# Optimization experiments

Hardware: AMD Instinct MI355X
Metric: run time of the kernel (lower is better)

The kernel has to match this reference:

```python
import jax, jax.numpy as jnp
import numpy as np
from jax import lax

DN = ('NCHW', 'OIHW', 'NCHW')


def _conv(x, w, b=None, pad='SAME'):
    y = lax.conv_general_dilated(x, w, (1, 1), pad, dimension_numbers=DN)
    return y if b is None else y + b[None, :, None, None]


def setup_inputs() -> dict:
    key = jax.random.key(0)
    ks = jax.random.split(key, 16)
    N, I, H, W = 8, 128, 40, 40
    C, Hc, A, P, O = 256, 256, 256, 256, 256  # in/hidden/attention/projection/out channels
    s = 0.05
    f32 = jnp.float32
    return {
        'x': jax.random.normal(ks[0], (N, I, H, W), f32),
        'h0': jax.random.normal(ks[1], (1, Hc, 1, 1), f32),
        'w_px': jax.random.normal(ks[2], (C, I, 1, 1), f32) * s,
        'b_px': jnp.zeros((C,), f32),
        'w_qx': jax.random.normal(ks[3], (A, C, 3, 3), f32) * s,
        'w_qh': jax.random.normal(ks[4], (A, Hc, 3, 3), f32) * s,
        'w_kx': jax.random.normal(ks[5], (A, C, 3, 3), f32) * (s * A ** -0.5),
        'w_kh': jax.random.normal(ks[6], (A, Hc, 3, 3), f32) * (s * A ** -0.5),
        'w_vx': jax.random.normal(ks[7], (P, C, 3, 3), f32) * s,
        'w_vh': jax.random.normal(ks[8], (P, Hc, 3, 3), f32) * s,
        'w_z': jax.random.normal(ks[9], (Hc, 2 * P, 1, 1), f32) * s,
        'b_z': jnp.ones((Hc,), f32),  # init_gate = 1
        'w_h': jax.random.normal(ks[10], (Hc, 2 * P, 1, 1), f32) * s,
        'b_h': jnp.zeros((Hc,), f32),
        'w_out': jax.random.normal(ks[11], (O, C + 2 * P, 1, 1), f32) * s,
        'b_out': jnp.zeros((O,), f32),
    }


def reference(x, h0, w_px, b_px, w_qx, w_qh, w_kx, w_kh, w_vx, w_vh,
              w_z, b_z, w_h, b_h, w_out, b_out):
    # proj_x: 1x1 conv fusing inputs (single input, groups=1)
    xp = _conv(x, w_px, b_px)
    N, _, H, W = xp.shape
    Q = H * W
    # x-side tokens are step-invariant: compute once
    q_x = _conv(xp, w_qx, pad='SAME').reshape(N, -1, Q)          # [N, A, Q]
    k_x4 = _conv(xp, w_kx, pad='VALID')                           # [N, A, H-2, W-2]
    D = k_x4.shape[2] * k_x4.shape[3]
    k_x = k_x4.reshape(N, -1, D)                                  # [N, A, D]
    v_x = _conv(xp, w_vx, pad='VALID').reshape(N, -1, D)          # [N, P, D]

    def step(h):
        q_h = _conv(h, w_qh, pad='SAME').reshape(N, -1, Q)
        k_h = _conv(h, w_kh, pad='VALID').reshape(N, -1, D)
        v_h = _conv(h, w_vh, pad='VALID').reshape(N, -1, D)
        q = jnp.stack([q_x, q_h], 0)   # [A=2(query src), N, C, Q]
        k = jnp.stack([k_x, k_h], 0)   # [B=2(key src),   N, C, D]
        v = jnp.stack([v_x, v_h], 0)   # [B=2,            N, P, D]
        logits = jnp.einsum('ancq,bncd->anbqd', q, k)   # [2, N, 2, Q, D]
        wt = jax.nn.softmax(logits, axis=-1)
        a = jnp.einsum('bncd,anbqd->anbcq', v, wt)       # [2, N, 2, P, Q]
        a = a.reshape(2, N, -1, H, W)                    # channel layout: (B, P)
        a_x, a_h = a[0], a[1]
        z = jax.nn.sigmoid(_conv(a_h, w_z, b_z))
        h_cand = jnp.tanh(_conv(a_h, w_h, b_h))
        h_new = z * h + (1.0 - z) * h_cand               # dropout p=0 -> identity
        out = _conv(jnp.concatenate([xp, a_x], axis=1), w_out, b_out)
        return out, h_new

    h = jnp.broadcast_to(h0, (N, h0.shape[1], H, W))
    _, h = step(h)          # step 1: builds hidden state
    out, _ = step(h)        # step 2: output depends on recurrent gate
    return out
```

## Files before the change

### kernel.cpp

```cpp
#include <hip/hip_runtime.h>
#include <math.h>


typedef _Float16 f16;
typedef _Float16 h8 __attribute__((ext_vector_type(8)));
typedef __attribute__((ext_vector_type(4))) float f4;

__device__ __forceinline__ ushort f2h(float f) {
  union { f16 h; ushort u; } cv; cv.h = (f16)f; return cv.u;
}
__device__ __forceinline__ float h2f(ushort u) {
  union { ushort u; f16 h; } cv; cv.u = u; return (float)cv.h;
}

struct MgArgs {
  const ushort* A; long sAb;
  const ushort* B; long sBb;
  int M, Nn, K, Krow, mode, gRow0, swap, aConv, bConv;
  const ushort* zp;
  float* Y; long sYb, sYm; int nPer; long sYb2;
  const float* bias; int biasN;
  ushort* Yh; long sYpb, sYpm, pOff;
  ushort* Y2h;
};

__device__ __forceinline__ void mg_body(const MgArgs& g, ushort* lbase)
{
  const int bz = blockIdx.z;
  const ushort* __restrict__ A = g.A + (long)bz * g.sAb;
  const ushort* __restrict__ B = g.B + (long)bz * g.sBb;
  const int mb = g.swap ? blockIdx.y : blockIdx.x;
  const int nb = g.swap ? blockIdx.x : blockIdx.y;
  const int m0 = mb * 64, n0 = nb * 64;
  const int t = threadIdx.x;
  const int lane = t & 63, wv = t >> 6;
  const int r = lane & 15, qd = lane >> 4;
  const int wn = wv * 16;
  const int lrow = lane >> 3, lch = lane & 7;
  f4 acc[4];
  #pragma unroll
  for (int i = 0; i < 4; ++i) acc[i] = (f4){0.f, 0.f, 0.f, 0.f};

  const int cg8 = (lch ^ lrow) * 8;
  int aB[2], aY[2], aX[2]; long aO[2];
  int bB[2], bY[2], bX[2]; long bO[2];
  #pragma unroll
  for (int i = 0; i < 2; ++i) {
    int gr = m0 + wv * 16 + i * 8 + lrow;
    if (g.aConv) {
      int n8 = gr / 1600, pos = gr - n8 * 1600;
      int py = pos / 40, px = pos - py * 40;
      aB[i] = n8 * 1600; aY[i] = py; aX[i] = px;
    } else { if (gr > g.M - 1) gr = g.M - 1; aO[i] = (long)gr * g.Krow; }
  }
  #pragma unroll
  for (int i = 0; i < 2; ++i) {
    int gr = n0 + wv * 16 + i * 8 + lrow;
    if (g.bConv) {
      int n8 = gr / 1600, pos = gr - n8 * 1600;
      int py = pos / 40, px = pos - py * 40;
      bB[i] = n8 * 1600; bY[i] = py; bX[i] = px;
    } else { if (gr > g.Nn - 1) gr = g.Nn - 1; bO[i] = (long)gr * g.Krow; }
  }

  auto stage = [&](int ch, int lb) {
    int cb = ch / 9, tap = ch - cb * 9;
    int tdy = tap / 3 - 1, tdx = tap - (tap / 3) * 3 - 1;
    int kin = cb << 6;
    int kc2 = ch << 6;
    #pragma unroll
    for (int i = 0; i < 2; ++i) {
      const ushort* p; size_t go;
      if (g.aConv) {
        int yy = aY[i] + tdy, xx = aX[i] + tdx;
        bool v = ((unsigned)yy < 40u) && ((unsigned)xx < 40u);
        if (v) { go = (size_t)(aB[i] + yy * 40 + xx) * 768 + kin + cg8; p = A; }
        else   { go = 0; p = g.zp; }
      } else { go = (size_t)(aO[i] + kc2 + cg8); p = A; }
      __builtin_amdgcn_global_load_lds(p + go, lbase + lb + wv * 1024 + i * 512, 16, 0, 0);
    }
    #pragma unroll
    for (int i = 0; i < 2; ++i) {
      const ushort* p; size_t go;
      if (g.bConv) {
        int yy = bY[i] + tdy, xx = bX[i] + tdx;
        bool v = ((unsigned)yy < 40u) && ((unsigned)xx < 40u);
        if (v) { go = (size_t)(bB[i] + yy * 40 + xx) * 768 + kin + cg8; p = B; }
        else   { go = 0; p = g.zp; }
      } else { go = (size_t)(bO[i] + kc2 + cg8); p = B; }
      __builtin_amdgcn_global_load_lds(p + go, lbase + lb + 4096 + wv * 1024 + i * 512, 16, 0, 0);
    }
  };

  auto compute = [&](int lb) {
    #pragma unroll
    for (int kk = 0; kk < 2; ++kk) {
      int off = (((kk << 2) + qd) ^ (r & 7)) << 3;
      h8 af[4], bf;
      #pragma unroll
      for (int mt = 0; mt < 4; ++mt)
        af[mt] = *(const h8*)&lbase[lb + (mt * 16 + r) * 64 + off];
      bf = *(const h8*)&lbase[lb + 4096 + (wn + r) * 64 + off];
      #pragma unroll
      for (int mt = 0; mt < 4; ++mt)
        acc[mt] = __builtin_amdgcn_mfma_f32_16x16x32_f16(af[mt], bf, acc[mt], 0, 0, 0);
    }
  };

  const int nch = g.K >> 6;
  stage(0, 0);
  int ch = 0;
  while (ch + 2 <= nch) {
    stage(ch + 1, 8192);
    asm volatile("s_waitcnt vmcnt(4)" ::: "memory");
    __builtin_amdgcn_s_barrier();
    __builtin_amdgcn_sched_barrier(0);
    compute(0);
    __builtin_amdgcn_s_barrier();
    __builtin_amdgcn_sched_barrier(0);
    if (ch + 2 < nch) {
      stage(ch + 2, 0);
      asm volatile("s_waitcnt vmcnt(4)" ::: "memory");
    } else {
      asm volatile("s_waitcnt vmcnt(0)" ::: "memory");
    }
    __builtin_amdgcn_s_barrier();
    __builtin_amdgcn_sched_barrier(0);
    compute(8192);
    __builtin_amdgcn_s_barrier();
    __builtin_amdgcn_sched_barrier(0);
    ch += 2;
  }
  if (ch < nch) {
    asm volatile("s_waitcnt vmcnt(0)" ::: "memory");
    __builtin_amdgcn_s_barrier();
    __builtin_amdgcn_sched_barrier(0);
    compute(0);
  }

  #pragma unroll
  for (int mt = 0; mt < 4; ++mt) {
    int nn = n0 + wn + r;
    if (nn >= g.Nn) continue;
    #pragma unroll
    for (int e = 0; e < 4; ++e) {
      int mm = m0 + mt * 16 + qd * 4 + e;
      if (mm >= g.M) continue;
      float v = acc[mt][e];
      if (g.mode == 0) {
        if (g.bias) v += g.bias[mm];
        int b2 = nn / g.nPer, nq = nn - b2 * g.nPer;
        g.Y[(size_t)bz * g.sYb + (size_t)b2 * g.sYb2 + (size_t)mm * g.sYm + nq] = v;
      } else if (g.mode == 1) {
        if (g.bias) v += g.bias[g.biasN ? nn : mm];
        g.Yh[(size_t)bz * g.sYpb + (size_t)mm * g.sYpm + nn + g.pOff] = f2h(v);
      } else if (g.mode == 2) {
        int gm = g.gRow0 + mm;
        int n8 = gm / 1600, q = gm - n8 * 1600;
        ushort h = f2h(v);
        if (nn < 256) {
          g.Yh[(size_t)n8 * 409600 + (size_t)q * 256 + nn] = h;
        } else {
          int qy = q / 40, qx = q - qy * 40;
          if (qy >= 1 && qy <= 38 && qx >= 1 && qx <= 38)
            g.Y2h[(size_t)n8 * 369664 + (size_t)((qy - 1) * 38 + qx - 1) * 256 + (nn - 256)] = h;
        }
      } else {
        int gn = g.gRow0 + nn;
        int n8 = gn / 1600, q = gn - n8 * 1600;
        int qy = q / 40, qx = q - qy * 40;
        if (qy >= 1 && qy <= 38 && qx >= 1 && qx <= 38)
          g.Yh[(size_t)n8 * 376832 + (size_t)mm * 1472 + (qy - 1) * 38 + qx - 1] = f2h(v);
      }
    }
  }
}

#define MG_KERN(name) \
__global__ __launch_bounds__(256) void name(MgArgs g) { \
  __shared__ ushort S[16384]; mg_body(g, S); }
MG_KERN(mg_xp)
MG_KERN(mg_v)
MG_KERN(mg_cls)
MG_KERN(mg_lg)
MG_KERN(mg_pv)
MG_KERN(mg_out)
#undef MG_KERN

__global__ __launch_bounds__(256) void mgemm_w(
    const ushort* __restrict__ A, long sAb,
    const ushort* __restrict__ B, long sBb,
    int M, int Nn, int K, int Krow, int mode, int gRow0, int swap,
    int aConv, int bConv,
    const ushort* __restrict__ zp,
    float* __restrict__ Y, long sYb, long sYm, int nPer, long sYb2,
    const float* __restrict__ bias, int biasN,
    ushort* __restrict__ Yh, long sYpb, long sYpm, long pOff,
    ushort* __restrict__ Y2h)
{
  __shared__ ushort S[12288];
  const int bz = blockIdx.z;
  A += (long)bz * sAb;
  B += (long)bz * sBb;
  const int mb = swap ? blockIdx.y : blockIdx.x;
  const int nb = swap ? blockIdx.x : blockIdx.y;
  const int m0 = mb * 64, n0 = nb * 128;
  const int t = threadIdx.x;
  const int lane = t & 63, wv = t >> 6;
  const int r = lane & 15, qd = lane >> 4;
  const int wn = wv * 32;
  const int lrow = lane >> 3, lch = lane & 7;
  f4 acc[4][2];
  #pragma unroll
  for (int i = 0; i < 4; ++i)
    #pragma unroll
    for (int j = 0; j < 2; ++j) acc[i][j] = (f4){0.f, 0.f, 0.f, 0.f};

  const int cg8 = (lch ^ lrow) * 8;
  int aB[2], aY[2], aX[2]; long aO[2];
  int bB[4], bY[4], bX[4]; long bO[4];
  #pragma unroll
  for (int i = 0; i < 2; ++i) {
    int gr = m0 + wv * 16 + i * 8 + lrow;
    if (aConv) {
      int n8 = gr / 1600, pos = gr - n8 * 1600;
      int py = pos / 40, px = pos - py * 40;
      aB[i] = n8 * 1600; aY[i] = py; aX[i] = px;
    } else { if (gr > M - 1) gr = M - 1; aO[i] = (long)gr * Krow; }
  }
  #pragma unroll
  for (int i = 0; i < 4; ++i) {
    int gr = n0 + wv * 32 + i * 8 + lrow;
    if (bConv) {
      int n8 = gr / 1600, pos = gr - n8 * 1600;
      int py = pos / 40, px = pos - py * 40;
      bB[i] = n8 * 1600; bY[i] = py; bX[i] = px;
    } else { if (gr > Nn - 1) gr = Nn - 1; bO[i] = (long)gr * Krow; }
  }

  ushort* lbase = S;
  for (int kc = 0; kc < K; kc += 64) {
    __syncthreads();
    int ch = kc >> 6;
    int cb = ch / 9, tap = ch - cb * 9;
    int tdy = tap / 3 - 1, tdx = tap - (tap / 3) * 3 - 1;
    int kin = cb << 6;
    #pragma unroll
    for (int i = 0; i < 2; ++i) {
      const ushort* p; size_t go;
      if (aConv) {
        int yy = aY[i] + tdy, xx = aX[i] + tdx;
        bool v = ((unsigned)yy < 40u) && ((unsigned)xx < 40u);
        if (v) { go = (size_t)(aB[i] + yy * 40 + xx) * 768 + kin + cg8; p = A; }
        else   { go = 0; p = zp; }
      } else { go = (size_t)(aO[i] + kc + cg8); p = A; }
      __builtin_amdgcn_global_load_lds(p + go, lbase + wv * 1024 + i * 512, 16, 0, 0);
    }
    #pragma unroll
    for (int i = 0; i < 4; ++i) {
      const ushort* p; size_t go;
      if (bConv) {
        int yy = bY[i] + tdy, xx = bX[i] + tdx;
        bool v = ((unsigned)yy < 40u) && ((unsigned)xx < 40u);
        if (v) { go = (size_t)(bB[i] + yy * 40 + xx) * 768 + kin + cg8; p = B; }
        else   { go = 0; p = zp; }
      } else { go = (size_t)(bO[i] + kc + cg8); p = B; }
      __builtin_amdgcn_global_load_lds(p + go, lbase + 4096 + wv * 2048 + i * 512, 16, 0, 0);
    }
    __syncthreads();
    #pragma unroll
    for (int kk = 0; kk < 2; ++kk) {
      int off = (((kk << 2) + qd) ^ (r & 7)) << 3;
      h8 af[4], bf[2];
      #pragma unroll
      for (int mt = 0; mt < 4; ++mt)
        af[mt] = *(const h8*)&lbase[(mt * 16 + r) * 64 + off];
      #pragma unroll
      for (int nt = 0; nt < 2; ++nt)
        bf[nt] = *(const h8*)&lbase[4096 + (wn + nt * 16 + r) * 64 + off];
      #pragma unroll
      for (int mt = 0; mt < 4; ++mt)
        #pragma unroll
        for (int nt = 0; nt < 2; ++nt)
          acc[mt][nt] = __builtin_amdgcn_mfma_f32_16x16x32_f16(af[mt], bf[nt], acc[mt][nt], 0, 0, 0);
    }
  }
  #pragma unroll
  for (int mt = 0; mt < 4; ++mt)
    #pragma unroll
    for (int nt = 0; nt < 2; ++nt) {
      int nn = n0 + wn + nt * 16 + r;
      if (nn >= Nn) continue;
      #pragma unroll
      for (int e = 0; e < 4; ++e) {
        int mm = m0 + mt * 16 + qd * 4 + e;
        if (mm >= M) continue;
        float v = acc[mt][nt][e];
        if (mode == 0) {
          if (bias) v += bias[mm];
          int b2 = nn / nPer, nq = nn - b2 * nPer;
          Y[(size_t)bz * sYb + (size_t)b2 * sYb2 + (size_t)mm * sYm + nq] = v;
        } else if (mode == 1) {
          if (bias) v += bias[biasN ? nn : mm];
          Yh[(size_t)bz * sYpb + (size_t)mm * sYpm + nn + pOff] = f2h(v);
        } else if (mode == 2) {
          int gm = gRow0 + mm;
          int n8 = gm / 1600, q = gm - n8 * 1600;
          ushort h = f2h(v);
          if (nn < 256) {
            Yh[(size_t)n8 * 409600 + (size_t)q * 256 + nn] = h;
          } else {
            int qy = q / 40, qx = q - qy * 40;
            if (qy >= 1 && qy <= 38 && qx >= 1 && qx <= 38)
              Y2h[(size_t)n8 * 369664 + (size_t)((qy - 1) * 38 + qx - 1) * 256 + (nn - 256)] = h;
          }
        } else {
          int gn = gRow0 + nn;
          int n8 = gn / 1600, q = gn - n8 * 1600;
          int qy = q / 40, qx = q - qy * 40;
          if (qy >= 1 && qy <= 38 && qx >= 1 && qx <= 38)
            Yh[(size_t)n8 * 376832 + (size_t)mm * 1472 + (qy - 1) * 38 + qx - 1] = f2h(v);
        }
      }
    }
}

__global__ __launch_bounds__(256) void prep_all(
    const float* __restrict__ x,
    const float* __restrict__ w_qx, const float* __restrict__ w_kx,
    const float* __restrict__ w_vx,
    const float* __restrict__ w_px, const float* __restrict__ w_out,
    const float* __restrict__ w_kh, const float* __restrict__ w_vh,
    const float* __restrict__ w_z, const float* __restrict__ w_h,
    ushort* __restrict__ xT, ushort* __restrict__ Wqk, ushort* __restrict__ Wv,
    ushort* __restrict__ wpx, ushort* __restrict__ wout,
    ushort* __restrict__ Wkv, ushort* __restrict__ Wzh,
    ushort* __restrict__ zp, ushort* __restrict__ vxp)
{
  long gi = (long)blockIdx.x * 256 + threadIdx.x;
  if (gi < 64) zp[gi] = 0;
  long i = gi;
  if (i < 1638400) {
    int i1 = (int)(i & 127); long r = i >> 7;
    int q = (int)(r % 1600); int n8 = (int)(r / 1600);
    xT[i] = f2h(x[(long)n8 * 204800 + (long)i1 * 1600 + q]);
    return;
  }
  i -= 1638400;
  if (i < 1769472) {
    int o = (int)(i / 2304), k = (int)(i - (long)o * 2304);
    int cb = k / 576, rem = k - cb * 576;
    int tap = rem >> 6, ci = rem & 63;
    int si = (cb * 64 + ci) * 9 + tap;
    float f; ushort* d; int oo;
    if (o < 256)      { f = w_qx[o * 2304 + si];         d = Wqk; oo = o; }
    else if (o < 512) { f = w_kx[(o - 256) * 2304 + si]; d = Wqk; oo = o; }
    else              { f = w_vx[(o - 512) * 2304 + si]; d = Wv;  oo = o - 512; }
    d[oo * 2304 + k] = f2h(f);
    return;
  }
  i -= 1769472;
  if (i < 32768)  { wpx[i]  = f2h(w_px[i]);  return; }
  i -= 32768;
  if (i < 196608) { wout[i] = f2h(w_out[i]); return; }
  i -= 196608;
  if (i < 1179648) { Wkv[i] = f2h(i < 589824 ? w_kh[i] : w_vh[i - 589824]); return; }
  i -= 1179648;
  if (i < 262144)  { Wzh[i] = f2h(i < 131072 ? w_z[i] : w_h[i - 131072]); return; }
  i -= 262144;
  if (i < 57344) {
    int j = (int)(i % 28); int rr = (int)(i / 28);
    int c = rr % 256, n = rr / 256;
    vxp[(size_t)n * 376832 + (size_t)c * 1472 + 1444 + j] = 0;
  }
}

__global__ __launch_bounds__(64) void uniform_kv_kern(
    const float* __restrict__ h0, const float* __restrict__ w_qh,
    const float* __restrict__ w_kh, const float* __restrict__ w_vh,
    float* __restrict__ qh1, float* __restrict__ kh1, float* __restrict__ vh1)
{
  int a = blockIdx.x, j = blockIdx.y, t = threadIdx.x;
  const float* wsel = (j < 9) ? w_qh : (j == 9) ? w_kh : w_vh;
  bool dyok0 = true, dyok2 = true, dxok0 = true, dxok2 = true;
  if (j < 9) {
    int uy = j / 3, ux = j - uy * 3;
    dyok0 = (uy != 0); dyok2 = (uy != 2);
    dxok0 = (ux != 0); dxok2 = (ux != 2);
  }
  float acc = 0.f;
  for (int c = t; c < 256; c += 64) {
    const float* wp = wsel + a * 2304 + c * 9;
    float s = 0.f;
    #pragma unroll
    for (int dy = 0; dy < 3; ++dy) {
      if ((dy == 0 && !dyok0) || (dy == 2 && !dyok2)) continue;
      #pragma unroll
      for (int dx = 0; dx < 3; ++dx) {
        if ((dx == 0 && !dxok0) || (dx == 2 && !dxok2)) continue;
        s += wp[dy * 3 + dx];
      }
    }
    acc += s * h0[c];
  }
  #pragma unroll
  for (int o = 32; o; o >>= 1) acc += __shfl_down(acc, o);
  if (t == 0) {
    if (j < 9) qh1[j * 256 + a] = acc;
    else if (j == 9) kh1[a] = acc;
    else vh1[a] = acc;
  }
}

__global__ __launch_bounds__(256) void l0_logits(
    const float* __restrict__ qh1, const ushort* __restrict__ kxT,
    float* __restrict__ L0)
{
  __shared__ float qs[2304];
  int db = blockIdx.x, n = blockIdx.y;
  for (int i = threadIdx.x; i < 2304; i += 256) qs[i] = qh1[i];
  __syncthreads();
  int d = db * 256 + threadIdx.x;
  bool act = d < 1444;
  const ushort* vp = kxT + (size_t)n * 369664 + (act ? (size_t)d * 256 : 0);
  float acc[9] = {0.f,0.f,0.f,0.f,0.f,0.f,0.f,0.f,0.f};
  for (int c8 = 0; c8 < 256; c8 += 8) {
    h8 v = *(const h8*)(const void*)(vp + c8);
    #pragma unroll
    for (int j = 0; j < 8; ++j) {
      float f = (float)v[j];
      #pragma unroll
      for (int u = 0; u < 9; ++u) acc[u] += qs[u * 256 + c8 + j] * f;
    }
  }
  if (act)
    for (int u = 0; u < 9; ++u) L0[n * 12996 + u * 1444 + d] = acc[u];
}

__global__ __launch_bounds__(256) void softmax_rows(float* __restrict__ p, int L)
{
  float* rp = p + (long)blockIdx.x * L;
  int t = threadIdx.x;
  __shared__ float redm[4], reds[4];
  float mx = -3.4e38f;
  for (int i = t; i < L; i += 256) mx = fmaxf(mx, rp[i]);
  #pragma unroll
  for (int o = 32; o; o >>= 1) mx = fmaxf(mx, __shfl_down(mx, o));
  if ((t & 63) == 0) redm[t >> 6] = mx;
  __syncthreads();
  mx = fmaxf(fmaxf(redm[0], redm[1]), fmaxf(redm[2], redm[3]));
  float s = 0.f;
  for (int i = t; i < L; i += 256) { float v = expf(rp[i] - mx); rp[i] = v; s += v; }
  #pragma unroll
  for (int o = 32; o; o >>= 1) s += __shfl_down(s, o);
  if ((t & 63) == 0) reds[t >> 6] = s;
  __syncthreads();
  float inv = 1.f / (reds[0] + reds[1] + reds[2] + reds[3]);
  for (int i = t; i < L; i += 256) rp[i] *= inv;
}

__global__ __launch_bounds__(256) void a10_pv(
    const float* __restrict__ L0, const ushort* __restrict__ vxp,
    float* __restrict__ a10)
{
  int u = blockIdx.x, n = blockIdx.y;
  __shared__ float wts[1472];
  const float* wrow = L0 + n * 12996 + u * 1444;
  for (int i = threadIdx.x; i < 1472; i += 256) wts[i] = (i < 1444) ? wrow[i] : 0.f;
  __syncthreads();
  int p = threadIdx.x;
  const ushort* vp = vxp + (size_t)n * 376832 + (size_t)p * 1472;
  float acc = 0.f;
  for (int d8 = 0; d8 < 1472; d8 += 8) {
    h8 v = *(const h8*)(const void*)(vp + d8);
    #pragma unroll
    for (int j = 0; j < 8; ++j) acc += wts[d8 + j] * (float)v[j];
  }
  a10[n * 2304 + u * 256 + p] = acc;
}

__global__ __launch_bounds__(256) void build_AV(
    const float* __restrict__ a10, const float* __restrict__ vh1,
    ushort* __restrict__ AV)
{
  int i = blockIdx.x * 256 + threadIdx.x;
  if (i >= 72 * 512) return;
  int row = i >> 9, j = i & 511;
  int n = row / 9, u = row - n * 9;
  float f = (j < 256) ? a10[n * 2304 + u * 256 + j] : vh1[j - 256];
  AV[i] = f2h(f);
}

__global__ __launch_bounds__(256) void gate_ew2(
    const float* __restrict__ pre72p, const float* __restrict__ b_z,
    const float* __restrict__ b_h, const float* __restrict__ h0,
    float* __restrict__ h1)
{
  int i = blockIdx.x * 256 + threadIdx.x;
  if (i >= 72 * 256) return;
  int row = i >> 8, c = i & 255;
  float zs = 0.f, hs = 0.f;
  #pragma unroll
  for (int s = 0; s < 4; ++s) {
    zs += pre72p[s * 36864 + row * 512 + c];
    hs += pre72p[s * 36864 + row * 512 + 256 + c];
  }
  float z = 1.f / (1.f + expf(-(zs + b_z[c])));
  float hv = tanhf(hs + b_h[c]);
  int n = row / 9, u = row - n * 9;
  h1[n * 2304 + c * 9 + u] = z * h0[c] + (1.f - z) * hv;
}

__global__ __launch_bounds__(256) void build_GA(
    const float* __restrict__ h1, ushort* __restrict__ GA)
{
  int i = blockIdx.x * 256 + threadIdx.x;
  if (i >= 72 * 2304) return;
  int row = i / 2304, k = i - row * 2304;
  int c = k / 9, tap = k - c * 9;
  int u = row % 9;
  int ty = u / 3, tx = u - ty * 3;
  int dy = tap / 3, dx = tap - dy * 3;
  int uy = (ty == 0) ? (dy == 0 ? 0 : 1) : (ty == 2) ? (dy == 2 ? 2 : 1) : 1;
  int ux = (tx == 0) ? (dx == 0 ? 0 : 1) : (tx == 2) ? (dx == 2 ? 2 : 1) : 1;
  GA[i] = f2h(h1[(row / 9) * 2304 + c * 9 + uy * 3 + ux]);
}

__global__ __launch_bounds__(256) void softmax_h16(
    const ushort* __restrict__ p, ushort* __restrict__ wt)
{
  long row = blockIdx.x;
  const ushort* rp = p + row * 1472;
  ushort* op = wt + row * 1472;
  int t = threadIdx.x;
  __shared__ float buf[1444];
  __shared__ float redm[4], reds[4];
  float mx = -3.4e38f;
  for (int i = t; i < 1444; i += 256) { float v = h2f(rp[i]); buf[i] = v; mx = fmaxf(mx, v); }
  #pragma unroll
  for (int o = 32; o; o >>= 1) mx = fmaxf(mx, __shfl_down(mx, o));
  if ((t & 63) == 0) redm[t >> 6] = mx;
  __syncthreads();
  mx = fmaxf(fmaxf(redm[0], redm[1]), fmaxf(redm[2], redm[3]));
  float s = 0.f;
  for (int i = t; i < 1444; i += 256) { float v = expf(buf[i] - mx); buf[i] = v; s += v; }
  #pragma unroll
  for (int o = 32; o; o >>= 1) s += __shfl_down(s, o);
  if ((t & 63) == 0) reds[t >> 6] = s;
  __syncthreads();
  float inv = 1.f / (reds[0] + reds[1] + reds[2] + reds[3]);
  for (int i = t; i < 1472; i += 256)
    op[i] = f2h((i < 1444) ? buf[i] * inv : 0.f);
}

__global__ __launch_bounds__(256) void attn_b1(
    const ushort* __restrict__ qT, const float* __restrict__ khvcp,
    ushort* __restrict__ xaT)
{
  __shared__ float ks[2304];
  __shared__ float vs[2304];
  __shared__ float es[256][10];
  int n = blockIdx.y;
  int q0 = blockIdx.x * 256;
  for (int i = threadIdx.x; i < 2304; i += 256) {
    int tt = i >> 8, c = i & 255;
    size_t base = (size_t)(n * 9 + tt) * 512;
    float sk = 0.f, sv = 0.f;
    #pragma unroll
    for (int s = 0; s < 6; ++s) {
      sk += khvcp[s * 36864 + base + c];
      sv += khvcp[s * 36864 + base + 256 + c];
    }
    ks[i] = sk; vs[i] = sv;
  }
  __syncthreads();
  int q = q0 + threadIdx.x;
  bool act = (q < 1600);
  float Lg[9] = {0.f,0.f,0.f,0.f,0.f,0.f,0.f,0.f,0.f};
  const ushort* qp = qT + (size_t)n * 409600 + (act ? (size_t)q * 256 : 0);
  for (int c8 = 0; c8 < 256; c8 += 8) {
    h8 v = *(const h8*)(const void*)(qp + c8);
    #pragma unroll
    for (int j = 0; j < 8; ++j) {
      float f = (float)v[j];
      #pragma unroll
      for (int tt = 0; tt < 9; ++tt) Lg[tt] += f * ks[tt * 256 + c8 + j];
    }
  }
  float mx = Lg[0];
  #pragma unroll
  for (int tt = 1; tt < 9; ++tt) mx = fmaxf(mx, Lg[tt]);
  float Z = 0.f;
  float e[9];
  #pragma unroll
  for (int tt = 0; tt < 9; ++tt) {
    float m = ((tt / 3) == 1 ? 36.f : 1.f) * ((tt % 3) == 1 ? 36.f : 1.f);
    e[tt] = act ? m * expf(Lg[tt] - mx) : 0.f;
    Z += e[tt];
  }
  float inv = act ? (1.f / Z) : 0.f;
  #pragma unroll
  for (int tt = 0; tt < 9; ++tt) es[threadIdx.x][tt] = e[tt] * inv;
  __syncthreads();
  int nact = 1600 - q0; if (nact > 256) nact = 256;
  int p = threadIdx.x;
  for (int qq = 0; qq < nact; ++qq) {
    float s = 0.f;
    #pragma unroll
    for (int tt = 0; tt < 9; ++tt) s += es[qq][tt] * vs[tt * 256 + p];
    xaT[(size_t)n * 1228800 + (size_t)(q0 + qq) * 768 + 512 + p] = f2h(s);
  }
}

extern "C" void kernel_launch(void* const* d_in, const int* in_sizes, int n_in,
                              void* d_out, int out_size, void* d_ws, size_t ws_size,
                              hipStream_t stream)
{
  const float* x     = (const float*)d_in[0];
  const float* h0    = (const float*)d_in[1];
  const float* w_px  = (const float*)d_in[2];
  const float* b_px  = (const float*)d_in[3];
  const float* w_qx  = (const float*)d_in[4];
  const float* w_qh  = (const float*)d_in[5];
  const float* w_kx  = (const float*)d_in[6];
  const float* w_kh  = (const float*)d_in[7];
  const float* w_vx  = (const float*)d_in[8];
  const float* w_vh  = (const float*)d_in[9];
  const float* w_z   = (const float*)d_in[10];
  const float* b_z   = (const float*)d_in[11];
  const float* w_h   = (const float*)d_in[12];
  const float* b_h   = (const float*)d_in[13];
  const float* w_out = (const float*)d_in[14];
  const float* b_out = (const float*)d_in[15];
  float* out = (float*)d_out;

  char* base = (char*)d_ws;
  size_t off = 0;
  auto alloc = [&](size_t bytes) -> char* {
    off = (off + 255) & ~(size_t)255;
    char* p = base + off; off += bytes; return p;
  };
  ushort* xaT   = (ushort*)alloc(19660800);
  ushort* qT    = (ushort*)alloc(6553600);
  ushort* kxT   = (ushort*)alloc(5914624);
  ushort* vxp   = (ushort*)alloc(6029312);
  ushort* xT    = (ushort*)alloc(3276800);
  ushort* Wqk   = (ushort*)alloc(2359296);
  ushort* Wv    = (ushort*)alloc(1179648);
  ushort* Wkv   = (ushort*)alloc(2359296);
  ushort* Wzh   = (ushort*)alloc(524288);
  ushort* wpx   = (ushort*)alloc(65536);
  ushort* wout  = (ushort*)alloc(393216);
  ushort* zp    = (ushort*)alloc(128);
  ushort* GA    = (ushort*)alloc(331776);
  ushort* AV    = (ushort*)alloc(73728);
  float*  pre72p= (float*)alloc(589824);
  float*  khvcp = (float*)alloc(884736);
  float*  qh1   = (float*)alloc(9216);
  float*  kh1   = (float*)alloc(1024);
  float*  vh1   = (float*)alloc(1024);
  float*  L0    = (float*)alloc(415872);
  float*  a10   = (float*)alloc(73728);
  float*  h1    = (float*)alloc(73728);
  off = (off + 255) & ~(size_t)255;
  char* chunk = base + off;
  long avail = (long)ws_size - (long)off;
  if (avail < 0) avail = 0;
  int an = (int)(avail / 9420800L); if (an < 1) an = 1; if (an > 8) an = 8;

  auto mk = [&](const ushort* A, long sAb, const ushort* B, long sBb,
                int M, int Nn, int K, int Krow, int mode, int gRow0, int swap,
                int aConv, int bConv,
                float* Y, long sYb, long sYm, int nPer, long sYb2,
                const float* bias, int biasN,
                ushort* Yh, long sYpb, long sYpm, long pOff, ushort* Y2h) {
    MgArgs g;
    g.A = A; g.sAb = sAb; g.B = B; g.sBb = sBb;
    g.M = M; g.Nn = Nn; g.K = K; g.Krow = Krow; g.mode = mode;
    g.gRow0 = gRow0; g.swap = swap; g.aConv = aConv; g.bConv = bConv;
    g.zp = zp;
    g.Y = Y; g.sYb = sYb; g.sYm = sYm; g.nPer = nPer; g.sYb2 = sYb2;
    g.bias = bias; g.biasN = biasN;
    g.Yh = Yh; g.sYpb = sYpb; g.sYpm = sYpm; g.pOff = pOff; g.Y2h = Y2h;
    return g;
  };
  const int BIG = 0x40000000;

  prep_all<<<dim3(20064), dim3(256), 0, stream>>>(
      x, w_qx, w_kx, w_vx, w_px, w_out, w_kh, w_vh, w_z, w_h,
      xT, Wqk, Wv, wpx, wout, Wkv, Wzh, zp, vxp);

  mg_xp<<<dim3(4, 200, 1), dim3(256), 0, stream>>>(mk(xT, 0, wpx, 0,
     12800, 256, 128, 128, 1, 0, 1, 0, 0,
     nullptr, 0, 0, 0, 0, b_px, 1,
     xaT, 0, 768, 0, nullptr));

  mgemm_w<<<dim3(4, 200, 1), dim3(256), 0, stream>>>(xaT, 0, Wqk, 0,
     12800, 512, 2304, 2304, 2, 0, 1, 1, 0, zp,
     nullptr, 0, 0, 0, 0, nullptr, 0,
     qT, 0, 0, 0, kxT);
  mg_v<<<dim3(4, 200, 1), dim3(256), 0, stream>>>(mk(Wv, 0, xaT, 0,
     256, 12800, 2304, 2304, 3, 0, 0, 0, 1,
     nullptr, 0, 0, 0, 0, nullptr, 0,
     vxp, 0, 0, 0, nullptr));

  uniform_kv_kern<<<dim3(256, 11), dim3(64), 0, stream>>>(h0, w_qh, w_kh, w_vh, qh1, kh1, vh1);
  l0_logits<<<dim3(6, 8), dim3(256), 0, stream>>>(qh1, kxT, L0);
  softmax_rows<<<dim3(72), dim3(256), 0, stream>>>(L0, 1444);
  a10_pv<<<dim3(9, 8), dim3(256), 0, stream>>>(L0, vxp, a10);
  build_AV<<<dim3(144), dim3(256), 0, stream>>>(a10, vh1, AV);
  mg_cls<<<dim3(2, 8, 4), dim3(256), 0, stream>>>(mk(AV, 128, Wzh, 128,
     72, 512, 128, 512, 0, 0, 0, 0, 0,
     pre72p, 36864, 512, BIG, 0, nullptr, 0,
     nullptr, 0, 0, 0, nullptr));
  gate_ew2<<<dim3(72), dim3(256), 0, stream>>>(pre72p, b_z, b_h, h0, h1);
  build_GA<<<dim3(648), dim3(256), 0, stream>>>(h1, GA);
  mg_cls<<<dim3(2, 8, 6), dim3(256), 0, stream>>>(mk(GA, 384, Wkv, 384,
     72, 512, 384, 2304, 0, 0, 0, 0, 0,
     khvcp, 36864, 512, BIG, 0, nullptr, 0,
     nullptr, 0, 0, 0, nullptr));
  attn_b1<<<dim3(7, 8), dim3(256), 0, stream>>>(qT, khvcp, xaT);

  {
    ushort* scL16 = (ushort*)chunk;
    for (int nb0 = 0; nb0 < 8; nb0 += an) {
      int c = (8 - nb0 < an) ? (8 - nb0) : an;
      ushort* wt = (ushort*)(chunk + (long)c * 4710400);
      mg_lg<<<dim3(25, 23, c), dim3(256), 0, stream>>>(mk(qT + (long)nb0 * 409600, 409600,
         kxT + (long)nb0 * 369664, 369664,
         1600, 1444, 256, 256, 1, 0, 0, 0, 0,
         nullptr, 0, 0, 0, 0, nullptr, 0,
         scL16, 2355200, 1472, 0, nullptr));
      softmax_h16<<<dim3(c * 1600), dim3(256), 0, stream>>>(scL16, wt);
      mg_pv<<<dim3(25, 4, c), dim3(256), 0, stream>>>(mk(wt, 2355200,
         vxp + (long)nb0 * 376832, 376832,
         1600, 256, 1472, 1472, 1, 0, 0, 0, 0,
         nullptr, 0, 0, 0, 0, nullptr, 0,
         xaT + (long)nb0 * 1228800, 1228800, 768, 256, nullptr));
    }
  }

  mg_out<<<dim3(4, 200, 1), dim3(256), 0, stream>>>(mk(wout, 0, xaT, 0,
     256, 12800, 768, 768, 0, 0, 0, 0, 0,
     out, 0, 1600, 1600, 409600, b_out, 0,
     nullptr, 0, 0, 0, nullptr));
}
```

Measured before the change: 436.6 us.

## Double-buffer LDS in the QK conv GEMM to overlap loads with MFMA

Turns the single-buffered K loop of the q/k conv GEMM into a two-stage ping-pong pipeline. The next 64-wide K chunk is issued with global_load_lds into a second LDS buffer while MFMAs run on the current one, using explicit vmcnt waits and barriers. This hides global-load latency that previously sat serialized between two syncthreads per chunk. LDS per block doubles, from 24 KB to 48 KB, which may cut occupancy, and the manual waitcnt counts must match the six loads issued per stage.

After: 471.1 us. 1.08x slower.

```diff
diff --git a/kernel.cpp b/kernel.cpp
--- a/kernel.cpp
+++ b/kernel.cpp
@@ -187,7 +187,7 @@
 MG_KERN(mg_out)
 #undef MG_KERN
 
-__global__ __launch_bounds__(256) void mgemm_w(
+__global__ __launch_bounds__(256) void mg_qk(
     const ushort* __restrict__ A, long sAb,
     const ushort* __restrict__ B, long sBb,
     int M, int Nn, int K, int Krow, int mode, int gRow0, int swap,
@@ -198,7 +198,7 @@
     ushort* __restrict__ Yh, long sYpb, long sYpm, long pOff,
     ushort* __restrict__ Y2h)
 {
-  __shared__ ushort S[12288];
+  __shared__ ushort S[24576];
   const int bz = blockIdx.z;
   A += (long)bz * sAb;
   B += (long)bz * sBb;
@@ -239,12 +239,12 @@
   }
 
   ushort* lbase = S;
-  for (int kc = 0; kc < K; kc += 64) {
-    __syncthreads();
-    int ch = kc >> 6;
+
+  auto stage = [&](int ch, int lb) {
     int cb = ch / 9, tap = ch - cb * 9;
     int tdy = tap / 3 - 1, tdx = tap - (tap / 3) * 3 - 1;
     int kin = cb << 6;
+    int kc2 = ch << 6;
     #pragma unroll
     for (int i = 0; i < 2; ++i) {
       const ushort* p; size_t go;
@@ -253,8 +253,8 @@
         bool v = ((unsigned)yy < 40u) && ((unsigned)xx < 40u);
         if (v) { go = (size_t)(aB[i] + yy * 40 + xx) * 768 + kin + cg8; p = A; }
         else   { go = 0; p = zp; }
-      } else { go = (size_t)(aO[i] + kc + cg8); p = A; }
-      __builtin_amdgcn_global_load_lds(p + go, lbase + wv * 1024 + i * 512, 16, 0, 0);
+      } else { go = (size_t)(aO[i] + kc2 + cg8); p = A; }
+      __builtin_amdgcn_global_load_lds(p + go, lbase + lb + wv * 1024 + i * 512, 16, 0, 0);
     }
     #pragma unroll
     for (int i = 0; i < 4; ++i) {
@@ -264,27 +264,61 @@
         bool v = ((unsigned)yy < 40u) && ((unsigned)xx < 40u);
         if (v) { go = (size_t)(bB[i] + yy * 40 + xx) * 768 + kin + cg8; p = B; }
         else   { go = 0; p = zp; }
-      } else { go = (size_t)(bO[i] + kc + cg8); p = B; }
-      __builtin_amdgcn_global_load_lds(p + go, lbase + 4096 + wv * 2048 + i * 512, 16, 0, 0);
-    }
-    __syncthreads();
+      } else { go = (size_t)(bO[i] + kc2 + cg8); p = B; }
+      __builtin_amdgcn_global_load_lds(p + go, lbase + lb + 4096 + wv * 2048 + i * 512, 16, 0, 0);
+    }
+  };
+
+  auto compute = [&](int lb) {
     #pragma unroll
     for (int kk = 0; kk < 2; ++kk) {
       int off = (((kk << 2) + qd) ^ (r & 7)) << 3;
       h8 af[4], bf[2];
       #pragma unroll
       for (int mt = 0; mt < 4; ++mt)
-        af[mt] = *(const h8*)&lbase[(mt * 16 + r) * 64 + off];
+        af[mt] = *(const h8*)&lbase[lb + (mt * 16 + r) * 64 + off];
       #pragma unroll
       for (int nt = 0; nt < 2; ++nt)
-        bf[nt] = *(const h8*)&lbase[4096 + (wn + nt * 16 + r) * 64 + off];
+        bf[nt] = *(const h8*)&lbase[lb + 4096 + (wn + nt * 16 + r) * 64 + off];
       #pragma unroll
       for (int mt = 0; mt < 4; ++mt)
         #pragma unroll
         for (int nt = 0; nt < 2; ++nt)
           acc[mt][nt] = __builtin_amdgcn_mfma_f32_16x16x32_f16(af[mt], bf[nt], acc[mt][nt], 0, 0, 0);
     }
-  }
+  };
+
+  const int nch = K >> 6;
+  stage(0, 0);
+  int ch = 0;
+  while (ch + 2 <= nch) {
+    stage(ch + 1, 12288);
+    asm volatile("s_waitcnt vmcnt(6)" ::: "memory");
+    __builtin_amdgcn_s_barrier();
+    __builtin_amdgcn_sched_barrier(0);
+    compute(0);
+    __builtin_amdgcn_s_barrier();
+    __builtin_amdgcn_sched_barrier(0);
+    if (ch + 2 < nch) {
+      stage(ch + 2, 0);
+      asm volatile("s_waitcnt vmcnt(6)" ::: "memory");
+    } else {
+      asm volatile("s_waitcnt vmcnt(0)" ::: "memory");
+    }
+    __builtin_amdgcn_s_barrier();
+    __builtin_amdgcn_sched_barrier(0);
+    compute(12288);
+    __builtin_amdgcn_s_barrier();
+    __builtin_amdgcn_sched_barrier(0);
+    ch += 2;
+  }
+  if (ch < nch) {
+    asm volatile("s_waitcnt vmcnt(0)" ::: "memory");
+    __builtin_amdgcn_s_barrier();
+    __builtin_amdgcn_sched_barrier(0);
+    compute(0);
+  }
+
   #pragma unroll
   for (int mt = 0; mt < 4; ++mt)
     #pragma unroll
@@ -695,7 +729,7 @@
      nullptr, 0, 0, 0, 0, b_px, 1,
      xaT, 0, 768, 0, nullptr));
 
-  mgemm_w<<<dim3(4, 200, 1), dim3(256), 0, stream>>>(xaT, 0, Wqk, 0,
+  mg_qk<<<dim3(4, 200, 1), dim3(256), 0, stream>>>(xaT, 0, Wqk, 0,
      12800, 512, 2304, 2304, 2, 0, 1, 1, 0, zp,
      nullptr, 0, 0, 0, 0, nullptr, 0,
      qT, 0, 0, 0, kxT);
```
